# Performance work log

Measured on AMD Instinct MI355X. Metric: run time of the kernel, lower is better.

The kernel has to match this reference:

```python
import jax, jax.numpy as jnp
import numpy as np

H = 1024     # hidden_size
NH = 16      # num heads
HD = H // NH # head_dim = 64
I = 4096     # intermediate_size
EPS = 1e-6


def rmsnorm(x, w, eps=EPS):
    var = jnp.mean(jnp.square(x), axis=-1, keepdims=True)
    return x * jax.lax.rsqrt(var + eps) * w


def attention(x, ctx, wq, wk, wv, wo):
    # x: [B,S,H], ctx: [B,Skv,H]; weights stored [in,out]
    B, S, _ = x.shape
    Skv = ctx.shape[1]
    q = (x @ wq).reshape(B, S, NH, HD)
    k = (ctx @ wk).reshape(B, Skv, NH, HD)
    v = (ctx @ wv).reshape(B, Skv, NH, HD)
    scores = jnp.einsum('bqhd,bkhd->bhqk', q, k) * (HD ** -0.5)
    attn = jax.nn.softmax(scores.astype(jnp.float32), axis=-1).astype(q.dtype)
    out = jnp.einsum('bhqk,bkhd->bqhd', attn, v).reshape(B, S, NH * HD)
    return out @ wo


def mlp(x, wg, wu, wd):
    return (jax.nn.silu(x @ wg) * (x @ wu)) @ wd


def setup_inputs() -> dict:
    key = jax.random.key(0)
    ks = jax.random.split(key, 16)
    p = lambda k, shape: (jax.random.normal(k, shape, jnp.float32) * 0.02)
    return {
        'hidden_states': jax.random.normal(ks[0], (1, 2048, H), jnp.float32),
        'context': jax.random.normal(ks[1], (1, 2048, H), jnp.float32),
        'sa_norm_w': jnp.ones((H,), jnp.float32),
        'sa_wq': p(ks[2], (H, NH * HD)),
        'sa_wk': p(ks[3], (H, NH * HD)),
        'sa_wv': p(ks[4], (H, NH * HD)),
        'sa_wo': p(ks[5], (NH * HD, H)),
        'ca_norm_w': jnp.ones((H,), jnp.float32),
        'ca_wq': p(ks[6], (H, NH * HD)),
        'ca_wk': p(ks[7], (H, NH * HD)),
        'ca_wv': p(ks[8], (H, NH * HD)),
        'ca_wo': p(ks[9], (NH * HD, H)),
        'mlp_norm_w': jnp.ones((H,), jnp.float32),
        'w_gate': p(ks[10], (H, I)),
        'w_up': p(ks[11], (H, I)),
        'w_down': p(ks[12], (I, H)),
    }


def reference(hidden_states, context, sa_norm_w, sa_wq, sa_wk, sa_wv, sa_wo,
              ca_norm_w, ca_wq, ca_wk, ca_wv, ca_wo,
              mlp_norm_w, w_gate, w_up, w_down):
    # self-attention block
    residual = hidden_states
    h = rmsnorm(hidden_states, sa_norm_w)
    h = residual + attention(h, h, sa_wq, sa_wk, sa_wv, sa_wo)
    # cross-attention block
    residual = h
    hn = rmsnorm(h, ca_norm_w)
    h = residual + attention(hn, context, ca_wq, ca_wk, ca_wv, ca_wo)
    # MLP block
    residual = h
    hn = rmsnorm(h, mlp_norm_w)
    h = residual + mlp(hn, w_gate, w_up, w_down)
    return h
```

## Files before the change

### kernel.cpp

```cpp
#include <hip/hip_runtime.h>

#define H 1024
#define S 2048
#define NH 16
#define HD 64
#define ISZ 4096

typedef __attribute__((ext_vector_type(8))) short s8v;
typedef __attribute__((ext_vector_type(4))) short s4v;
typedef __attribute__((ext_vector_type(4))) float f4v;
typedef __attribute__((ext_vector_type(2))) unsigned u2v;

__device__ __forceinline__ short f2bf(float f) {
    unsigned u = __builtin_bit_cast(unsigned, f);
    unsigned r = (u + 0x7FFFu + ((u >> 16) & 1u)) >> 16;
    return (short)r;
}
__device__ __forceinline__ float bf2f(short s) {
    unsigned u = ((unsigned)(unsigned short)s) << 16;
    return __builtin_bit_cast(float, u);
}
__device__ __forceinline__ float exp2_hw(float x) {
    float r; asm("v_exp_f32 %0, %1" : "=v"(r) : "v"(x)); return r;
}
__device__ __forceinline__ unsigned cvt_pk_bf16(float lo, float hi) {
    unsigned r; asm("v_cvt_pk_bf16_f32 %0, %1, %2" : "=v"(r) : "v"(lo), "v"(hi)); return r;
}

__device__ __forceinline__ void gload_lds16(const short* g, short* l) {
    __builtin_amdgcn_global_load_lds(
        (const __attribute__((address_space(1))) void*)g,
        (__attribute__((address_space(3))) void*)l, 16, 0, 0);
}

struct PreArgs {
    const void* hid; const void* ctx;
    const void* sanw; const void* canw; const void* mlpnw;
    const void* w[11];
    short* hidc; short* ctxc; short* xn;
    short* canw_o; short* mlpnw_o;
    short* wT[11];
    int* flag_out;
};

__device__ __forceinline__ void tr_tile(const void* src, short* dst, int K, int N,
                                        int k0, int n0, int rmul, int roff,
                                        int isbf, float* tile ) {
    int t = threadIdx.x;
    int c = t & 31, r0 = t >> 5;
    if (isbf) {
        const short* s = (const short*)src;
#pragma unroll
        for (int i = 0; i < 4; i++)
            tile[(r0 + i * 8) * 33 + c] = bf2f(s[(k0 + r0 + i * 8) * N + n0 + c]);
    } else {
        const float* s = (const float*)src;
#pragma unroll
        for (int i = 0; i < 4; i++)
            tile[(r0 + i * 8) * 33 + c] = s[(k0 + r0 + i * 8) * N + n0 + c];
    }
    __syncthreads();
#pragma unroll
    for (int i = 0; i < 4; i++)
        dst[((n0 + r0 + i * 8) * rmul + roff) * K + k0 + c] = f2bf(tile[c * 33 + r0 + i * 8]);
}

__global__ __launch_bounds__(256) void preamble_kernel(PreArgs pa) {
    __shared__ float tile[32 * 33];
    __shared__ float red[4];
    int b = blockIdx.x;
    int t = threadIdx.x;
    int isbf = (((const unsigned*)pa.sanw)[0] == 0x3F803F80u);
    if (blockIdx.x == 0 && t == 0) pa.flag_out[0] = isbf;

    if (b < 2048) {
        int row = b;
        float xf[4];
        if (isbf) {
            s4v xv = *(const s4v*)((const short*)pa.hid + row * H + t * 4);
#pragma unroll
            for (int j = 0; j < 4; j++) xf[j] = bf2f(xv[j]);
        } else {
            const float* s = (const float*)pa.hid + row * H + t * 4;
#pragma unroll
            for (int j = 0; j < 4; j++) xf[j] = s[j];
        }
        float ss = 0.f;
        s4v cv;
#pragma unroll
        for (int j = 0; j < 4; j++) { cv[j] = f2bf(xf[j]); xf[j] = bf2f(cv[j]); ss += xf[j] * xf[j]; }
        *(s4v*)(pa.hidc + row * H + t * 4) = cv;
        int lane = t & 63, wid = t >> 6;
#pragma unroll
        for (int off = 32; off >= 1; off >>= 1) ss += __shfl_xor(ss, off);
        if (lane == 0) red[wid] = ss;
        __syncthreads();
        float tot = red[0] + red[1] + red[2] + red[3];
        float scale = rsqrtf(tot * (1.f / (float)H) + 1e-6f);
        float wv[4];
        if (isbf) {
            s4v wq = *(const s4v*)((const short*)pa.sanw + t * 4);
#pragma unroll
            for (int j = 0; j < 4; j++) wv[j] = bf2f(wq[j]);
        } else {
            const float* s = (const float*)pa.sanw + t * 4;
#pragma unroll
            for (int j = 0; j < 4; j++) wv[j] = s[j];
        }
        s4v ov;
#pragma unroll
        for (int j = 0; j < 4; j++) ov[j] = f2bf(xf[j] * scale * wv[j]);
        *(s4v*)(pa.xn + row * H + t * 4) = ov;
        return;
    }
    b -= 2048;
    if (b < 1024) {
        int i8 = b * 2048 + t * 8;
        if (isbf) {
            *(s8v*)(pa.ctxc + i8) = *(const s8v*)((const short*)pa.ctx + i8);
        } else {
            const float* s = (const float*)pa.ctx;
            s8v o;
#pragma unroll
            for (int j = 0; j < 8; j++) o[j] = f2bf(s[i8 + j]);
            *(s8v*)(pa.ctxc + i8) = o;
        }
        return;
    }
    b -= 1024;
    if (b < 2) {
        const void* src = (b == 0) ? pa.canw : pa.mlpnw;
        short* dst = (b == 0) ? pa.canw_o : pa.mlpnw_o;
        if (isbf) { if (t * 4 < H) *(s4v*)(dst + t * 4) = *(const s4v*)((const short*)src + t * 4); }
        else {
            const float* s = (const float*)src;
            s4v o;
#pragma unroll
            for (int j = 0; j < 4; j++) o[j] = f2bf(s[t * 4 + j]);
            *(s4v*)(dst + t * 4) = o;
        }
        return;
    }
    b -= 2;
    if (b < 8 * 1024) {
        int w = b >> 10, tl = b & 1023;
        tr_tile(pa.w[w], pa.wT[w], H, H, (tl & 31) * 32, (tl >> 5) * 32, 1, 0, isbf, tile);
        return;
    }
    b -= 8 * 1024;
    if (b < 2 * 4096) {
        int w = 8 + (b >> 12), tl = b & 4095;
        tr_tile(pa.w[w], pa.wT[8], H, ISZ, (tl & 31) * 32, (tl >> 5) * 32, 2, w - 8, isbf, tile);
        return;
    }
    b -= 2 * 4096;
    {
        tr_tile(pa.w[10], pa.wT[10], ISZ, H, (b & 127) * 32, (b >> 7) * 32, 1, 0, isbf, tile);
    }
}

__global__ __launch_bounds__(256) void rmsnorm_kernel(const short* __restrict__ x,
                                                      const short* __restrict__ w,
                                                      short* __restrict__ out) {
    int row = blockIdx.x;
    int t = threadIdx.x;
    int lane = t & 63, wid = t >> 6;
    const short* xr = x + row * H;

    s4v xv = *(const s4v*)(xr + t * 4);
    float xf[4];
    float ss = 0.f;
#pragma unroll
    for (int j = 0; j < 4; j++) { xf[j] = bf2f(xv[j]); ss += xf[j] * xf[j]; }
#pragma unroll
    for (int off = 32; off >= 1; off >>= 1) ss += __shfl_xor(ss, off);

    __shared__ float red[4];
    if (lane == 0) red[wid] = ss;
    __syncthreads();
    float tot = red[0] + red[1] + red[2] + red[3];
    float scale = rsqrtf(tot * (1.f / (float)H) + 1e-6f);

    s4v wv = *(const s4v*)(w + t * 4);
    s4v ov;
#pragma unroll
    for (int j = 0; j < 4; j++) ov[j] = f2bf(xf[j] * scale * bf2f(wv[j]));
    *(s4v*)(out + row * H + t * 4) = ov;
}

template <int BM_, int BN_>
__global__ __launch_bounds__(512, 2) void gemm_bt_kernel(
    const short* __restrict__ A0, const short* __restrict__ A1, int split, int lda,
    const short* __restrict__ Bt,
    void* __restrict__ C, int ldc, int K,
    const short* __restrict__ res,
    const int* __restrict__ dtype_flag,
    short* __restrict__ vtbuf, int vcol0,
    short* __restrict__ silu_out) {

    constexpr int MC = BM_ / 32;
    constexpr int NC = BN_ / 64;
    constexpr int U  = (BM_ + BN_) / 8;
    constexpr int PT = U / 8;
    constexpr int BUF = (BM_ + BN_) * 64;

    __shared__ short lds[2 * BUF];

    const short* A = (blockIdx.y < split) ? A0 : A1;
    int m0 = blockIdx.x * BM_;
    int n0 = blockIdx.y * BN_;

    int t = threadIdx.x;
    int lane = t & 63, wid = t >> 6;
    int quad = lane >> 4, l15 = lane & 15;
    int wr = wid >> 2, wc = wid & 3;
    int ld4 = lane >> 2, lc8 = (lane & 3) * 8;

    f4v acc[MC][NC] = {};

    auto stage = [&](short* buf, int k0) {
#pragma unroll
        for (int s = 0; s < PT; ++s) {
            int u = wid * PT + s;
            if (u < BM_ / 8) {
                int h = u / (BM_ / 16), r16 = u % (BM_ / 16);
                gload_lds16(A + (m0 + r16 * 16 + ld4) * lda + k0 + h * 32 + lc8,
                            buf + h * (BM_ * 32) + r16 * 512);
            } else {
                int ub = u - BM_ / 8;
                int h = ub / (BN_ / 16), r16 = ub % (BN_ / 16);
                gload_lds16(Bt + (n0 + r16 * 16 + ld4) * K + k0 + h * 32 + lc8,
                            buf + BM_ * 64 + h * (BN_ * 32) + r16 * 512);
            }
        }
    };

    auto compute = [&](const short* buf) {
#pragma unroll
        for (int kh = 0; kh < 2; ++kh) {
            s8v af[MC], bfv[NC];
#pragma unroll
            for (int mc = 0; mc < MC; ++mc)
                af[mc] = *(const s8v*)(buf + kh * (BM_ * 32) +
                                       (wr * (BM_ / 2) + mc * 16 + l15) * 32 + quad * 8);
#pragma unroll
            for (int nc = 0; nc < NC; ++nc)
                bfv[nc] = *(const s8v*)(buf + BM_ * 64 + kh * (BN_ * 32) +
                                        (wc * (BN_ / 4) + nc * 16 + l15) * 32 + quad * 8);
#pragma unroll
            for (int mc = 0; mc < MC; ++mc)
#pragma unroll
                for (int nc = 0; nc < NC; ++nc)
                    acc[mc][nc] = __builtin_amdgcn_mfma_f32_16x16x32_bf16(af[mc], bfv[nc], acc[mc][nc], 0, 0, 0);
        }
    };

    const int KT = K / 64;
    stage(lds, 0);
    __syncthreads();
    int cur = 0;
    for (int kt = 0; kt < KT - 1; ++kt) {
        stage(lds + (cur ^ 1) * BUF, (kt + 1) * 64);
        compute(lds + cur * BUF);
        __syncthreads();
        cur ^= 1;
    }
    compute(lds + cur * BUF);

    if (silu_out) {
#pragma unroll
        for (int mc = 0; mc < MC; mc++) {
#pragma unroll
            for (int nc = 0; nc < NC; nc++) {
                int row = m0 + wr * (BM_ / 2) + mc * 16 + quad * 4;
                int col = n0 + wc * (BN_ / 4) + nc * 16 + l15;
#pragma unroll
                for (int r = 0; r < 4; r++) {
                    float v = acc[mc][nc][r];
                    float other = __shfl_xor(v, 1);
                    if ((l15 & 1) == 0) {
                        float sig = 1.f / (1.f + __expf(-v));
                        silu_out[(row + r) * ISZ + (col >> 1)] = f2bf(v * sig * other);
                    }
                }
            }
        }
        return;
    }

    int out_fp32 = (dtype_flag != nullptr) && (dtype_flag[0] == 0);

#pragma unroll
    for (int mc = 0; mc < MC; mc++) {
#pragma unroll
        for (int nc = 0; nc < NC; nc++) {
            int row = m0 + wr * (BM_ / 2) + mc * 16 + quad * 4;
            int col = n0 + wc * (BN_ / 4) + nc * 16 + l15;
#pragma unroll
            for (int r = 0; r < 4; r++) {
                float vf = acc[mc][nc][r];
                if (res) vf += bf2f(res[(row + r) * ldc + col]);
                if (vtbuf && col >= vcol0)
                    vtbuf[(col - vcol0) * S + row + r] = f2bf(vf);
                else if (out_fp32)
                    ((float*)C)[(row + r) * ldc + col] = vf;
                else
                    ((short*)C)[(row + r) * ldc + col] = f2bf(vf);
            }
        }
    }
}

__global__ __launch_bounds__(512, 4) void flash_attn_kernel(const short* __restrict__ q,
                                                            const short* __restrict__ kk,
                                                            const short* __restrict__ vt,
                                                            int rs,
                                                            short* __restrict__ o) {
    __shared__ short lds[40960];

    int h = blockIdx.y;
    int q0 = blockIdx.x * 64;
    int t = threadIdx.x;
    int lane = t & 63, wid = t >> 6;
    int quad = lane >> 4, l15 = lane & 15;
    int gw = wid & 3, gh = wid >> 2;
    int kvbase = gh * 1024;
    int kro = l15 & 7;

    int lrow = lane >> 3;
    int lsrc = ((lane & 7) ^ lrow) * 8;

    auto stageKV = [&](int buf, int tt) {
        int kvt = kvbase + tt * 64;
        short* kb = lds + (gh * 2 + buf) * 4096;
        short* vb = lds + 16384 + (gh * 2 + buf) * 4096;
#pragma unroll
        for (int i = 0; i < 2; i++) {
            int r0 = gw * 16 + i * 8;
            gload_lds16(kk + (kvt + r0 + lrow) * rs + h * HD + lsrc, kb + r0 * 64);
            gload_lds16(vt + (h * HD + r0 + lrow) * S + kvt + lsrc, vb + r0 * 64);
        }
    };

    const float qscale = 0.125f * 1.44269504f;
    s8v bq[2];
    int qrow = q0 + gw * 16 + l15;
#pragma unroll
    for (int c = 0; c < 2; c++) {
        s8v raw = *(const s8v*)(q + qrow * rs + h * HD + c * 32 + quad * 8);
#pragma unroll
        for (int j = 0; j < 8; j++) bq[c][j] = f2bf(qscale * bf2f(raw[j]));
    }

    f4v o_acc[4] = {};
    float m_s = -INFINITY, l_s = 0.f;
    short* pw = lds + 32768 + wid * 1024;

    const int NT = 16;
    stageKV(0, 0);
    __syncthreads();
    int cur = 0;
    for (int tt = 0; tt < NT; ++tt) {
        if (tt + 1 < NT) stageKV(cur ^ 1, tt + 1);
        const short* kb = lds + (gh * 2 + cur) * 4096;
        const short* vb = lds + 16384 + (gh * 2 + cur) * 4096;

        f4v st[4];
#pragma unroll
        for (int kc = 0; kc < 4; kc++) {
            f4v a_ = (f4v){0.f, 0.f, 0.f, 0.f};
#pragma unroll
            for (int dc = 0; dc < 2; dc++) {
                s8v kf = *(const s8v*)(kb + (kc * 16 + l15) * 64 + ((dc * 4 + quad) ^ kro) * 8);
                a_ = __builtin_amdgcn_mfma_f32_16x16x32_bf16(kf, bq[dc], a_, 0, 0, 0);
            }
            st[kc] = a_;
        }

        float mloc = -INFINITY;
#pragma unroll
        for (int kc = 0; kc < 4; kc++)
#pragma unroll
            for (int r = 0; r < 4; r++) mloc = fmaxf(mloc, st[kc][r]);
        mloc = fmaxf(mloc, __shfl_xor(mloc, 16));
        mloc = fmaxf(mloc, __shfl_xor(mloc, 32));
        float m_new = fmaxf(m_s, mloc);
        float alpha = exp2_hw(m_s - m_new);
        float lloc = 0.f;
#pragma unroll
        for (int kc = 0; kc < 4; kc++)
#pragma unroll
            for (int r = 0; r < 4; r++) {
                float p = exp2_hw(st[kc][r] - m_new);
                st[kc][r] = p;
                lloc += p;
            }
        lloc += __shfl_xor(lloc, 16);
        lloc += __shfl_xor(lloc, 32);
        l_s = l_s * alpha + lloc;
        m_s = m_new;
#pragma unroll
        for (int nd = 0; nd < 4; nd++)
#pragma unroll
            for (int r = 0; r < 4; r++) o_acc[nd][r] *= alpha;

#pragma unroll
        for (int kc = 0; kc < 4; kc++) {
            u2v w;
            w[0] = cvt_pk_bf16(st[kc][0], st[kc][1]);
            w[1] = cvt_pk_bf16(st[kc][2], st[kc][3]);
            int pslot = (kc * 2 + (quad >> 1)) ^ kro;
            *(u2v*)(pw + l15 * 64 + pslot * 8 + (quad & 1) * 4) = w;
        }

#pragma unroll
        for (int nd = 0; nd < 4; nd++) {
#pragma unroll
            for (int kc2 = 0; kc2 < 2; kc2++) {
                s8v vf = *(const s8v*)(vb + (nd * 16 + l15) * 64 + ((kc2 * 4 + quad) ^ kro) * 8);
                s8v pf = *(const s8v*)(pw + l15 * 64 + ((kc2 * 4 + quad) ^ kro) * 8);
                o_acc[nd] = __builtin_amdgcn_mfma_f32_16x16x32_bf16(vf, pf, o_acc[nd], 0, 0, 0);
            }
        }
        __syncthreads();
        cur ^= 1;
    }

    float* ex = (float*)lds;
    if (gh == 1) {
        int base = (gw * 64 + lane) * 20;
#pragma unroll
        for (int nd = 0; nd < 4; nd++) *(f4v*)(ex + base + nd * 4) = o_acc[nd];
        ex[base + 16] = m_s;
        ex[base + 17] = l_s;
    }
    __syncthreads();
    if (gh == 1) return;

    int base = (wid * 64 + lane) * 20;
    float mB = ex[base + 16], lB = ex[base + 17];
    float M = fmaxf(m_s, mB);
    float a = exp2_hw(m_s - M), bsc = exp2_hw(mB - M);
    float inv = 1.f / (a * l_s + bsc * lB);
#pragma unroll
    for (int nd = 0; nd < 4; nd++) {
        f4v ob = *(const f4v*)(ex + base + nd * 4);
#pragma unroll
        for (int r = 0; r < 4; r++)
            o_acc[nd][r] = (a * o_acc[nd][r] + bsc * ob[r]) * inv;
    }

#pragma unroll
    for (int nd = 0; nd < 4; nd++)
#pragma unroll
        for (int r = 0; r < 4; r++)
            pw[l15 * 64 + nd * 16 + quad * 4 + r] = f2bf(o_acc[nd][r]);

    int qr = lane >> 2, dc2 = (lane & 3) * 16;
    s8v x0 = *(const s8v*)(pw + qr * 64 + dc2);
    s8v x1 = *(const s8v*)(pw + qr * 64 + dc2 + 8);
    short* dst = o + (q0 + wid * 16 + qr) * H + h * HD + dc2;
    *(s8v*)(dst) = x0;
    *(s8v*)(dst + 8) = x1;
}

extern "C" void kernel_launch(void* const* d_in, const int* in_sizes, int n_in,
                              void* d_out, int out_size, void* d_ws, size_t ws_size,
                              hipStream_t stream) {
    const int SH = S * H;
    const int WH = H * H;
    const int WI = H * ISZ;

    int* flag = (int*)d_ws;
    short* base = (short*)d_ws + 16;

    short* hidc   = base;
    short* ctxc   = hidc + SH;
    short* sanw   = ctxc + SH;
    short* canw   = sanw + H;
    short* mlpnw  = canw + H;
    short* saqkvT = mlpnw + H;
    short* sawoT  = saqkvT + 3 * WH;
    short* caqkvT = sawoT + WH;
    short* cawoT  = caqkvT + 3 * WH;
    short* wguT   = cawoT + WH;
    short* wdT    = wguT + 2 * WI;
    short* xn     = wdT + WI;
    short* qkv    = xn + SH;
    short* ao     = qkv + 3 * SH;
    short* h1     = ao + SH;
    short* gu     = qkv;
    short* h2     = qkv + 8 * SH;
    short* vt     = h2 + SH;

    dim3 blk(256);
    dim3 blk2(512);

    PreArgs pa;
    pa.hid = d_in[0]; pa.ctx = d_in[1];
    pa.sanw = d_in[2]; pa.canw = d_in[7]; pa.mlpnw = d_in[12];
    const void* wsrc[11] = {d_in[3], d_in[4], d_in[5], d_in[6],
                            d_in[8], d_in[9], d_in[10], d_in[11],
                            d_in[13], d_in[14], d_in[15]};
    short* wdst[11] = {saqkvT, saqkvT + WH, saqkvT + 2 * WH, sawoT,
                       caqkvT, caqkvT + WH, caqkvT + 2 * WH, cawoT,
                       wguT, wguT , wdT};
    for (int i = 0; i < 11; i++) { pa.w[i] = wsrc[i]; pa.wT[i] = wdst[i]; }
    pa.hidc = hidc; pa.ctxc = ctxc; pa.xn = xn;
    pa.canw_o = canw; pa.mlpnw_o = mlpnw;
    pa.flag_out = flag;
    const int pre_blocks = 2048 + 1024 + 2 + 8 * 1024 + 2 * 4096 + 4096;
    preamble_kernel<<<pre_blocks, blk, 0, stream>>>(pa);

    gemm_bt_kernel<128, 128><<<dim3(S / 128, 3 * H / 128), blk2, 0, stream>>>(
        xn, xn, 24, H, saqkvT, qkv, 3 * H, H, nullptr, nullptr, vt, 2 * H, nullptr);
    flash_attn_kernel<<<dim3(S / 64, NH), blk2, 0, stream>>>(qkv, qkv + H, vt, 3 * H, ao);
    gemm_bt_kernel<64, 128><<<dim3(S / 64, H / 128), blk2, 0, stream>>>(
        ao, ao, 8, H, sawoT, h1, H, H, hidc, nullptr, nullptr, 0, nullptr);

    rmsnorm_kernel<<<S, blk, 0, stream>>>(h1, canw, xn);
    gemm_bt_kernel<128, 128><<<dim3(S / 128, 3 * H / 128), blk2, 0, stream>>>(
        xn, ctxc, 8, H, caqkvT, qkv, 3 * H, H, nullptr, nullptr, vt, 2 * H, nullptr);
    flash_attn_kernel<<<dim3(S / 64, NH), blk2, 0, stream>>>(qkv, qkv + H, vt, 3 * H, ao);
    gemm_bt_kernel<64, 128><<<dim3(S / 64, H / 128), blk2, 0, stream>>>(
        ao, ao, 8, H, cawoT, h2, H, H, h1, nullptr, nullptr, 0, nullptr);

    rmsnorm_kernel<<<S, blk, 0, stream>>>(h2, mlpnw, xn);
    gemm_bt_kernel<256, 256><<<dim3(S / 256, 2 * ISZ / 256), blk2, 0, stream>>>(
        xn, xn, 32, H, wguT, nullptr, 2 * ISZ, H, nullptr, nullptr, nullptr, 0, gu);
    gemm_bt_kernel<64, 128><<<dim3(S / 64, H / 128), blk2, 0, stream>>>(
        gu, gu, 8, ISZ, wdT, d_out, H, ISZ, h2, flag, nullptr, 0, nullptr);
}
```

Measured before the change: 458.6 us.

## Add dedicated gate-up GEMM kernel with phased LDS pipelining and block swizzle

Replaces the generic 256x256 gemm_bt launch for the MLP gate/up projection with a specialized kernel. The new kernel splits each 64-wide K step into four quarter-phases, interleaving async global-to-LDS loads of the next tile with MFMA work under barriers, partial vmcnt waits and s_setprio raised around MFMA bursts. It also remaps the block index to group blocks that share weight tiles for better L2 reuse, and fuses SiLU(gate)*up in the epilogue using lane shuffles. In exchange it adds more barriers and a hard-coded 1024-wide K and tile layout, and the epilogue assumes interleaved gate/up columns.

```diff
diff --git a/kernel.cpp b/kernel.cpp
--- a/kernel.cpp
+++ b/kernel.cpp
@@ -10,6 +10,8 @@
 typedef __attribute__((ext_vector_type(4))) short s4v;
 typedef __attribute__((ext_vector_type(4))) float f4v;
 typedef __attribute__((ext_vector_type(2))) unsigned u2v;
+
+#define MFMA16 __builtin_amdgcn_mfma_f32_16x16x32_bf16
 
 __device__ __forceinline__ short f2bf(float f) {
     unsigned u = __builtin_bit_cast(unsigned, f);
@@ -251,7 +253,7 @@
             for (int mc = 0; mc < MC; ++mc)
 #pragma unroll
                 for (int nc = 0; nc < NC; ++nc)
-                    acc[mc][nc] = __builtin_amdgcn_mfma_f32_16x16x32_bf16(af[mc], bfv[nc], acc[mc][nc], 0, 0, 0);
+                    acc[mc][nc] = MFMA16(af[mc], bfv[nc], acc[mc][nc], 0, 0, 0);
         }
     };
 
@@ -311,6 +313,161 @@
     }
 }
 
+__global__ __launch_bounds__(512, 2) void gemm_gu8_kernel(
+    const short* __restrict__ A, const short* __restrict__ Bt,
+    short* __restrict__ silu_out) {
+
+    __shared__ short lds[65536];
+
+    int lin = blockIdx.x;
+    int sw = (lin & 7) * 32 + (lin >> 3);
+    int m0 = (sw & 7) * 256;
+    int n0 = (sw >> 3) * 256;
+
+    int t = threadIdx.x;
+    int lane = t & 63, wid = t >> 6;
+    int quad = lane >> 4, l15 = lane & 15;
+    int wr = wid >> 2, wc = wid & 3;
+    int ld4 = lane >> 2, lc8 = (lane & 3) * 8;
+
+    f4v acc[8][4] = {};
+
+    const short* Arow = A + (m0 + ld4) * 1024 + lc8;
+    const short* Brow = Bt + (n0 + ld4) * 1024 + lc8;
+
+    auto stA = [&](int buf, int kt, int kh) {
+        short* d = lds + buf * 32768 + kh * 8192;
+#pragma unroll
+        for (int i = 0; i < 2; i++) {
+            int r0 = (wid + 8 * i) * 16;
+            gload_lds16(Arow + r0 * 1024 + kt * 64 + kh * 32, d + r0 * 32);
+        }
+    };
+    auto stB = [&](int buf, int kt, int kh) {
+        short* d = lds + buf * 32768 + 16384 + kh * 8192;
+#pragma unroll
+        for (int i = 0; i < 2; i++) {
+            int r0 = (wid + 8 * i) * 16;
+            gload_lds16(Brow + r0 * 1024 + kt * 64 + kh * 32, d + r0 * 32);
+        }
+    };
+
+    const int aoff = (wr * 128 + l15) * 32 + quad * 8;
+    const int boff = 16384 + (wc * 64 + l15) * 32 + quad * 8;
+
+    stA(0, 0, 0); stB(0, 0, 0); stA(0, 0, 1); stB(0, 0, 1);
+    asm volatile("s_waitcnt vmcnt(4)" ::: "memory");
+    __builtin_amdgcn_s_barrier();
+
+    int cur = 0;
+    for (int kt = 0; kt < 15; ++kt) {
+        const short* bc = lds + cur * 32768;
+        int nb = cur ^ 1;
+        s8v af[8], b0, b1;
+
+#pragma unroll
+        for (int mc = 0; mc < 8; ++mc) af[mc] = *(const s8v*)(bc + aoff + mc * 512);
+        b0 = *(const s8v*)(bc + boff);
+        b1 = *(const s8v*)(bc + boff + 512);
+        stA(nb, kt + 1, 0);
+        __builtin_amdgcn_s_barrier();
+        asm volatile("s_waitcnt lgkmcnt(0)" ::: "memory");
+        __builtin_amdgcn_s_setprio(1);
+#pragma unroll
+        for (int mc = 0; mc < 8; ++mc) {
+            acc[mc][0] = MFMA16(af[mc], b0, acc[mc][0], 0, 0, 0);
+            acc[mc][1] = MFMA16(af[mc], b1, acc[mc][1], 0, 0, 0);
+        }
+        __builtin_amdgcn_s_setprio(0);
+        __builtin_amdgcn_s_barrier();
+
+        b0 = *(const s8v*)(bc + boff + 1024);
+        b1 = *(const s8v*)(bc + boff + 1536);
+        stB(nb, kt + 1, 0);
+        asm volatile("s_waitcnt vmcnt(4)" ::: "memory");
+        __builtin_amdgcn_s_barrier();
+        asm volatile("s_waitcnt lgkmcnt(0)" ::: "memory");
+        __builtin_amdgcn_s_setprio(1);
+#pragma unroll
+        for (int mc = 0; mc < 8; ++mc) {
+            acc[mc][2] = MFMA16(af[mc], b0, acc[mc][2], 0, 0, 0);
+            acc[mc][3] = MFMA16(af[mc], b1, acc[mc][3], 0, 0, 0);
+        }
+        __builtin_amdgcn_s_setprio(0);
+        __builtin_amdgcn_s_barrier();
+
+#pragma unroll
+        for (int mc = 0; mc < 8; ++mc) af[mc] = *(const s8v*)(bc + 8192 + aoff + mc * 512);
+        b0 = *(const s8v*)(bc + 8192 + boff);
+        b1 = *(const s8v*)(bc + 8192 + boff + 512);
+        stA(nb, kt + 1, 1);
+        __builtin_amdgcn_s_barrier();
+        asm volatile("s_waitcnt lgkmcnt(0)" ::: "memory");
+        __builtin_amdgcn_s_setprio(1);
+#pragma unroll
+        for (int mc = 0; mc < 8; ++mc) {
+            acc[mc][0] = MFMA16(af[mc], b0, acc[mc][0], 0, 0, 0);
+            acc[mc][1] = MFMA16(af[mc], b1, acc[mc][1], 0, 0, 0);
+        }
+        __builtin_amdgcn_s_setprio(0);
+        __builtin_amdgcn_s_barrier();
+
+        b0 = *(const s8v*)(bc + 8192 + boff + 1024);
+        b1 = *(const s8v*)(bc + 8192 + boff + 1536);
+        stB(nb, kt + 1, 1);
+        asm volatile("s_waitcnt vmcnt(4)" ::: "memory");
+        __builtin_amdgcn_s_barrier();
+        asm volatile("s_waitcnt lgkmcnt(0)" ::: "memory");
+        __builtin_amdgcn_s_setprio(1);
+#pragma unroll
+        for (int mc = 0; mc < 8; ++mc) {
+            acc[mc][2] = MFMA16(af[mc], b0, acc[mc][2], 0, 0, 0);
+            acc[mc][3] = MFMA16(af[mc], b1, acc[mc][3], 0, 0, 0);
+        }
+        __builtin_amdgcn_s_setprio(0);
+        __builtin_amdgcn_s_barrier();
+
+        cur ^= 1;
+    }
+
+    asm volatile("s_waitcnt vmcnt(0)" ::: "memory");
+    __builtin_amdgcn_s_barrier();
+    {
+        const short* bc = lds + cur * 32768;
+#pragma unroll
+        for (int kh = 0; kh < 2; ++kh) {
+            s8v af[8], bv[4];
+#pragma unroll
+            for (int mc = 0; mc < 8; ++mc) af[mc] = *(const s8v*)(bc + kh * 8192 + aoff + mc * 512);
+#pragma unroll
+            for (int nc = 0; nc < 4; ++nc) bv[nc] = *(const s8v*)(bc + kh * 8192 + boff + nc * 512);
+#pragma unroll
+            for (int mc = 0; mc < 8; ++mc)
+#pragma unroll
+                for (int nc = 0; nc < 4; ++nc)
+                    acc[mc][nc] = MFMA16(af[mc], bv[nc], acc[mc][nc], 0, 0, 0);
+        }
+    }
+
+#pragma unroll
+    for (int mc = 0; mc < 8; mc++) {
+#pragma unroll
+        for (int nc = 0; nc < 4; nc++) {
+            int row = m0 + wr * 128 + mc * 16 + quad * 4;
+            int col = n0 + wc * 64 + nc * 16 + l15;
+#pragma unroll
+            for (int r = 0; r < 4; r++) {
+                float v = acc[mc][nc][r];
+                float other = __shfl_xor(v, 1);
+                if ((l15 & 1) == 0) {
+                    float sig = 1.f / (1.f + __expf(-v));
+                    silu_out[(row + r) * ISZ + (col >> 1)] = f2bf(v * sig * other);
+                }
+            }
+        }
+    }
+}
+
 __global__ __launch_bounds__(512, 4) void flash_attn_kernel(const short* __restrict__ q,
                                                             const short* __restrict__ kk,
                                                             const short* __restrict__ vt,
@@ -372,7 +529,7 @@
 #pragma unroll
             for (int dc = 0; dc < 2; dc++) {
                 s8v kf = *(const s8v*)(kb + (kc * 16 + l15) * 64 + ((dc * 4 + quad) ^ kro) * 8);
-                a_ = __builtin_amdgcn_mfma_f32_16x16x32_bf16(kf, bq[dc], a_, 0, 0, 0);
+                a_ = MFMA16(kf, bq[dc], a_, 0, 0, 0);
             }
             st[kc] = a_;
         }
@@ -419,7 +576,7 @@
             for (int kc2 = 0; kc2 < 2; kc2++) {
                 s8v vf = *(const s8v*)(vb + (nd * 16 + l15) * 64 + ((kc2 * 4 + quad) ^ kro) * 8);
                 s8v pf = *(const s8v*)(pw + l15 * 64 + ((kc2 * 4 + quad) ^ kro) * 8);
-                o_acc[nd] = __builtin_amdgcn_mfma_f32_16x16x32_bf16(vf, pf, o_acc[nd], 0, 0, 0);
+                o_acc[nd] = MFMA16(vf, pf, o_acc[nd], 0, 0, 0);
             }
         }
         __syncthreads();
@@ -526,8 +683,7 @@
         ao, ao, 8, H, cawoT, h2, H, H, h1, nullptr, nullptr, 0, nullptr);
 
     rmsnorm_kernel<<<S, blk, 0, stream>>>(h2, mlpnw, xn);
-    gemm_bt_kernel<256, 256><<<dim3(S / 256, 2 * ISZ / 256), blk2, 0, stream>>>(
-        xn, xn, 32, H, wguT, nullptr, 2 * ISZ, H, nullptr, nullptr, nullptr, 0, gu);
+    gemm_gu8_kernel<<<dim3(256), blk2, 0, stream>>>(xn, wguT, gu);
     gemm_bt_kernel<64, 128><<<dim3(S / 64, H / 128), blk2, 0, stream>>>(
         gu, gu, 8, ISZ, wdT, d_out, H, ISZ, h2, flag, nullptr, 0, nullptr);
 }
```

Result: faster. 443.5 us (-3.3%).
